# Kernel optimization log

Hardware: AMD Instinct MI355X
Metric: run time of the kernel (lower is better)

The kernel has to match this reference:

```python
import jax, jax.numpy as jnp
import numpy as np

B, T, F, H, K = 64, 256, 16, 128, 3


def setup_inputs() -> dict:
    key = jax.random.key(0)
    ks = jax.random.split(key, 8)
    s = 1.0 / np.sqrt(H)
    x = jax.random.normal(ks[0], (B, T, F), jnp.float32)
    index = jnp.sort(jax.random.randint(ks[1], (B, 2), 0, T), axis=1)
    # per-feature LSTM params (input dim 1), torch gate order [i, f, g, o]
    W_ih = jax.random.uniform(ks[2], (F, 4 * H), jnp.float32, -s, s)
    W_hh = jax.random.uniform(ks[3], (F, 4 * H, H), jnp.float32, -s, s)
    b = jax.random.uniform(ks[4], (F, 4 * H), jnp.float32, -s, s)  # b_ih + b_hh folded
    conv_w = jax.random.uniform(ks[5], (K,), jnp.float32, -1.0 / np.sqrt(K), 1.0 / np.sqrt(K))
    fc_w = jax.random.uniform(ks[6], (F * H, 2), jnp.float32, -1.0 / np.sqrt(F * H), 1.0 / np.sqrt(F * H))
    fc_b = jax.random.uniform(ks[7], (2,), jnp.float32, -1.0 / np.sqrt(F * H), 1.0 / np.sqrt(F * H))
    return dict(x=x, index=index, W_ih=W_ih, W_hh=W_hh, b=b, conv_w=conv_w, fc_w=fc_w, fc_b=fc_b)


def reference(x, index, W_ih, W_hh, b, conv_w, fc_w, fc_b):
    Bn, Tn, Fn = x.shape
    Hn = W_hh.shape[-1]
    t = jnp.arange(Tn)
    # valid[b, t] = start <= t < end; recurrence only advances inside the ragged slice
    valid = (t[None, :] >= index[:, 0:1]) & (t[None, :] < index[:, 1:2])  # [B, T]
    xs = jnp.moveaxis(x, 1, 0)            # [T, B, F]
    ms = jnp.moveaxis(valid, 1, 0)[:, :, None, None]  # [T, B, 1, 1]

    def step(carry, inp):
        h, c = carry                       # [B, F, H] each
        x_t, m = inp                       # [B, F], [B, 1, 1]
        gates = x_t[:, :, None] * W_ih[None] \
            + jnp.einsum('bfh,fgh->bfg', h, W_hh) + b[None]  # [B, F, 4H]
        i, f, g, o = jnp.split(gates, 4, axis=-1)
        i = jax.nn.sigmoid(i); f = jax.nn.sigmoid(f)
        g = jnp.tanh(g); o = jax.nn.sigmoid(o)
        c_new = f * c + i * g
        h_new = o * jnp.tanh(c_new)
        h = jnp.where(m, h_new, h)
        c = jnp.where(m, c_new, c)
        return (h, c), None

    h0 = jnp.zeros((Bn, Fn, Hn), x.dtype)
    (h, _), _ = jax.lax.scan(step, (h0, h0), (xs, ms))
    outs = h                               # [B, F, H] == last LSTM output per slice

    cofs = outs.mean(axis=-1)              # AdaptiveAvgPool1d(1) -> [B, F]
    cofs = jax.lax.conv_general_dilated(
        cofs[:, None, :], conv_w[None, None, :], (1,), [(K // 2, K // 2)],
        dimension_numbers=('NCH', 'OIH', 'NCH'))[:, 0, :]  # [B, F]
    gate = jax.nn.sigmoid(cofs)
    outs = outs * gate[:, :, None]
    return outs.reshape(Bn, -1) @ fc_w + fc_b  # [B, 2]
```

## Files before the change

### kernel.cpp

```cpp
#include <hip/hip_runtime.h>

typedef _Float16 half_t;
typedef half_t half2_t __attribute__((ext_vector_type(2)));
typedef half_t half8  __attribute__((ext_vector_type(8)));
typedef unsigned int uint_t;
typedef uint_t uint4v __attribute__((ext_vector_type(4)));
typedef float float4v __attribute__((ext_vector_type(4)));

#define B_  64
#define T_  256
#define F_  16
#define H_  128
#define HP  160
#define LOG2E 1.44269504f

__device__ __forceinline__ float rcp_(float x)  { return __builtin_amdgcn_rcpf(x); }
__device__ __forceinline__ float sigm2(float x) { return rcp_(1.0f + __builtin_amdgcn_exp2f(x * -LOG2E)); }
__device__ __forceinline__ float tanh2(float x) { return fmaf(rcp_(1.0f + __builtin_amdgcn_exp2f(x * (-2.0f * LOG2E))), 2.0f, -1.0f); }
__device__ __forceinline__ float sigm(float x)  { return rcp_(1.0f + __expf(-x)); }

__global__ void make_sched(const int* __restrict__ index, int* __restrict__ pairs) {
    __shared__ int ss[B_], ee[B_], mid[B_], bo[B_];
    const int t = threadIdx.x;
    const int s = index[2 * t], e = index[2 * t + 1];
    ss[t] = s; ee[t] = e; mid[t] = s + e;
    __syncthreads();
    int m = mid[t], r = 0;
    for (int j = 0; j < B_; ++j) r += (mid[j] < m) || (mid[j] == m && j < t);
    bo[r] = t;
    __syncthreads();
    if (t < 32) {
        int bA = bo[2 * t], bB = bo[2 * t + 1];
        int su = min(ss[bA], ss[bB]), eu = max(ee[bA], ee[bB]);
        int4 v;
        v.x = (bA << 8) | bB;
        v.y = (ss[bA] << 16) | ee[bA];
        v.z = (ss[bB] << 16) | ee[bB];
        v.w = (su << 16) | eu;
        ((int4*)pairs)[t] = v;
    }
}

__global__ void repack_w(const float* __restrict__ whh, uint_t* __restrict__ wt) {
    const int f = blockIdx.x, w = blockIdx.y, tid = threadIdx.x;
    const int lane = tid & 63, q4 = tid >> 6;
    const int li = lane & 15, lg = lane >> 4;
    const float* base = whh + (size_t)f * 512 * 128;
#pragma unroll
    for (int qq = 0; qq < 4; ++qq) {
        const int qf = q4 * 4 + qq;
        const int m = qf >> 2, kt = qf & 3;
        const int g512 = 128 * m + 16 * w + li;
        uint_t tmp[4];
#pragma unroll
        for (int e2 = 0; e2 < 4; ++e2) {
            int k = kt * 32 + lg * 8 + 2 * e2;
            half2_t h;
            h[0] = (half_t)base[g512 * 128 + k];
            h[1] = (half_t)base[g512 * 128 + k + 1];
            tmp[e2] = __builtin_bit_cast(uint_t, h);
        }
        uint4 out = { tmp[0], tmp[1], tmp[2], tmp[3] };
        ((uint4*)wt)[(((size_t)f * 8 + w) * 16 + qf) * 64 + lane] = out;
    }
}

__global__ __launch_bounds__(512, 4) void lstm_mfma(
    const float* __restrict__ x, const uint_t* __restrict__ wt,
    const float* __restrict__ wih_g, const float* __restrict__ bias_g,
    const int* __restrict__ pairs, float* __restrict__ hout)
{
    __shared__ float xsh[2][T_ + 8];
    __shared__ alignas(16) half_t hbuf[2][2][HP];

    const int f = blockIdx.x & 15;
    const int4 pv = ((const int4*)pairs)[blockIdx.x >> 4];
    const int bA = pv.x >> 8, bB = pv.x & 255;
    const int sA = pv.y >> 16, eA = pv.y & 0xffff;
    const int sB = pv.z >> 16, eB = pv.z & 0xffff;
    const int su = pv.w >> 16, eu = pv.w & 0xffff;

    const int tid = threadIdx.x, lane = tid & 63, w = tid >> 6;
    const int li = lane & 15, lg = lane >> 4;
    const int cell = 16 * w + li;
    const int hsel = li >> 3;
    const int csel = lg >> 1;

    uint4v wr[16];
    {
        const char* ws = (const char*)wt + ((((size_t)f * 8 + w) * 16) * 64 + lane) * 16;
#pragma unroll
        for (int q = 0; q < 16; ++q) {
            unsigned long long a = (unsigned long long)(ws + (size_t)q * 1024);
            asm volatile("global_load_dwordx4 %0, %1, off" : "=v"(wr[q]) : "v"(a));
        }
        asm volatile("s_waitcnt vmcnt(0)");
        __builtin_amdgcn_sched_barrier(0);
    }

    float wih[4], bb4[4];
#pragma unroll
    for (int m = 0; m < 4; ++m) {
        wih[m] = wih_g[f * 512 + 128 * m + cell];
        bb4[m] = bias_g[f * 512 + 128 * m + cell];
    }

    const int myb = csel ? bB : bA;
    const int mys = csel ? sB : sA;
    const int mye = csel ? eB : eA;

    {
        int bb_ = tid >> 8, tt = tid & 255;
        xsh[bb_][tt] = x[((size_t)(bb_ ? bB : bA) * T_ + tt) * F_ + f];
    }
    if (tid < 2 * H_) hbuf[0][tid >> 7][tid & 127] = (half_t)0.0f;

    float cst = 0.0f, hst = 0.0f;
    int pp = 0;
    __syncthreads();

    for (int t = su; t < eu; ++t) {
        const half_t* hb = &hbuf[pp][hsel][lg * 8];
        half8 a0 = *(const half8*)(hb + 0);
        half8 a1 = *(const half8*)(hb + 32);
        half8 a2 = *(const half8*)(hb + 64);
        half8 a3 = *(const half8*)(hb + 96);
        float xt = xsh[csel][t];

        float gv[4];
#pragma unroll
        for (int m = 0; m < 4; ++m) {
            float iv = fmaf(xt, wih[m], bb4[m]);
            float4v ci = { iv, iv, iv, iv };
            ci = __builtin_amdgcn_mfma_f32_16x16x32_f16(a0, __builtin_bit_cast(half8, wr[m * 4 + 0]), ci, 0, 0, 0);
            ci = __builtin_amdgcn_mfma_f32_16x16x32_f16(a1, __builtin_bit_cast(half8, wr[m * 4 + 1]), ci, 0, 0, 0);
            ci = __builtin_amdgcn_mfma_f32_16x16x32_f16(a2, __builtin_bit_cast(half8, wr[m * 4 + 2]), ci, 0, 0, 0);
            ci = __builtin_amdgcn_mfma_f32_16x16x32_f16(a3, __builtin_bit_cast(half8, wr[m * 4 + 3]), ci, 0, 0, 0);
            gv[m] = ci[0];
        }

        float gi = sigm2(gv[0]);
        float gf = sigm2(gv[1]);
        float gg = tanh2(gv[2]);
        float go = sigm2(gv[3]);
        float cn = fmaf(gf, cst, gi * gg);
        bool mk = (t >= mys) & (t < mye);
        cst = mk ? cn : cst;
        float hn = go * tanh2(cst);
        hst = mk ? hn : hst;

        if ((lg & 1) == 0) hbuf[pp ^ 1][csel][cell] = (half_t)hst;
        __syncthreads();
        pp ^= 1;
    }

    if ((lg & 1) == 0) hout[((size_t)myb * F_ + f) * H_ + cell] = hst;
}

__global__ void epilogue(const float* __restrict__ hout, const float* __restrict__ conv_w,
                         const float* __restrict__ fc_w, const float* __restrict__ fc_b,
                         float* __restrict__ out)
{
    const int b = blockIdx.x, t = threadIdx.x;
    const int lane = t & 63, wv = t >> 6;
    __shared__ float part[2][16];
    __shared__ float gate_sh[16];

    float hv[16];
#pragma unroll
    for (int f = 0; f < 16; ++f) hv[f] = hout[((size_t)b * 16 + f) * 128 + t];

#pragma unroll
    for (int f = 0; f < 16; ++f) {
        float s = hv[f];
#pragma unroll
        for (int off = 32; off >= 1; off >>= 1) s += __shfl_down(s, off, 64);
        if (lane == 0) part[wv][f] = s;
    }
    __syncthreads();
    if (t < 16) gate_sh[t] = (part[0][t] + part[1][t]) * (1.0f / 128.0f);
    __syncthreads();
    float gate = 0.0f;
    if (t < 16) {
        float l  = (t > 0)  ? gate_sh[t - 1] : 0.0f;
        float mi = gate_sh[t];
        float r  = (t < 15) ? gate_sh[t + 1] : 0.0f;
        gate = sigm(fmaf(l, conv_w[0], fmaf(mi, conv_w[1], r * conv_w[2])));
    }
    __syncthreads();
    if (t < 16) gate_sh[t] = gate;
    __syncthreads();

    float acc0 = 0.0f, acc1 = 0.0f;
    const float2* fw2 = (const float2*)fc_w;
#pragma unroll
    for (int f = 0; f < 16; ++f) {
        float hg = hv[f] * gate_sh[f];
        float2 w2 = fw2[f * 128 + t];
        acc0 = fmaf(hg, w2.x, acc0);
        acc1 = fmaf(hg, w2.y, acc1);
    }
#pragma unroll
    for (int off = 32; off >= 1; off >>= 1) {
        acc0 += __shfl_down(acc0, off, 64);
        acc1 += __shfl_down(acc1, off, 64);
    }
    if (lane == 0) { part[wv][0] = acc0; part[wv][1] = acc1; }
    __syncthreads();
    if (t == 0) {
        out[b * 2 + 0] = part[0][0] + part[1][0] + fc_b[0];
        out[b * 2 + 1] = part[0][1] + part[1][1] + fc_b[1];
    }
}

extern "C" void kernel_launch(void* const* d_in, const int* in_sizes, int n_in,
                              void* d_out, int out_size, void* d_ws, size_t ws_size,
                              hipStream_t stream) {
    const float* x      = (const float*)d_in[0];
    const int*   index  = (const int*)  d_in[1];
    const float* W_ih   = (const float*)d_in[2];
    const float* W_hh   = (const float*)d_in[3];
    const float* bias   = (const float*)d_in[4];
    const float* conv_w = (const float*)d_in[5];
    const float* fc_w   = (const float*)d_in[6];
    const float* fc_b   = (const float*)d_in[7];
    float* out = (float*)d_out;

    uint_t* wt    = (uint_t*)d_ws;
    float*  hout  = (float*)((char*)d_ws + 2 * 1024 * 1024);
    int*    pairs = (int*)((char*)d_ws + 2 * 1024 * 1024 + 512 * 1024);

    make_sched<<<1, 64, 0, stream>>>(index, pairs);
    repack_w<<<dim3(F_, 8), 256, 0, stream>>>(W_hh, wt);
    lstm_mfma<<<512, 512, 0, stream>>>(x, wt, W_ih, bias, pairs, hout);
    epilogue<<<B_, 128, 0, stream>>>(hout, conv_w, fc_w, fc_b, out);
}
```

Measured before the change: 136.0 us.

## Halve LSTM block size by giving each wave two cell tiles

Each block now runs 4 waves instead of 8, and each wave handles two 16-cell column tiles, holding twice as many weight registers and issuing 32 MFMAs per step. The input and bias term is added after the MFMA chain instead of seeding the accumulator. Every lane then writes a distinct hidden value, so no lanes sit idle on the store. The aim is to cut the per-step barrier cost, since fewer waves synchronise each timestep. In exchange each wave does twice the serial MFMA and activation work, register pressure rises, and occupancy may drop.

```diff
diff --git a/kernel.cpp b/kernel.cpp
--- a/kernel.cpp
+++ b/kernel.cpp
@@ -65,7 +65,7 @@
     }
 }
 
-__global__ __launch_bounds__(512, 4) void lstm_mfma(
+__global__ __launch_bounds__(256, 2) void lstm_mfma(
     const float* __restrict__ x, const uint_t* __restrict__ wt,
     const float* __restrict__ wih_g, const float* __restrict__ bias_g,
     const int* __restrict__ pairs, float* __restrict__ hout)
@@ -82,40 +82,50 @@
 
     const int tid = threadIdx.x, lane = tid & 63, w = tid >> 6;
     const int li = lane & 15, lg = lane >> 4;
-    const int cell = 16 * w + li;
     const int hsel = li >> 3;
     const int csel = lg >> 1;
-
-    uint4v wr[16];
+    const int sub  = lg & 1;
+    const int cell0 = 16 * w + li;
+    const int wcell = cell0 + 64 * sub;
+
+    uint4v wr[2][16];
     {
-        const char* ws = (const char*)wt + ((((size_t)f * 8 + w) * 16) * 64 + lane) * 16;
-#pragma unroll
-        for (int q = 0; q < 16; ++q) {
-            unsigned long long a = (unsigned long long)(ws + (size_t)q * 1024);
-            asm volatile("global_load_dwordx4 %0, %1, off" : "=v"(wr[q]) : "v"(a));
+#pragma unroll
+        for (int cb = 0; cb < 2; ++cb) {
+            const char* ws = (const char*)wt + ((((size_t)f * 8 + (w + 4 * cb)) * 16) * 64 + lane) * 16;
+#pragma unroll
+            for (int q = 0; q < 16; ++q) {
+                unsigned long long a = (unsigned long long)(ws + (size_t)q * 1024);
+                asm volatile("global_load_dwordx4 %0, %1, off" : "=v"(wr[cb][q]) : "v"(a));
+            }
         }
         asm volatile("s_waitcnt vmcnt(0)");
         __builtin_amdgcn_sched_barrier(0);
     }
 
-    float wih[4], bb4[4];
-#pragma unroll
-    for (int m = 0; m < 4; ++m) {
-        wih[m] = wih_g[f * 512 + 128 * m + cell];
-        bb4[m] = bias_g[f * 512 + 128 * m + cell];
-    }
+    float wih[2][4], bb4[2][4];
+#pragma unroll
+    for (int cb = 0; cb < 2; ++cb)
+#pragma unroll
+        for (int m = 0; m < 4; ++m) {
+            wih[cb][m] = wih_g[f * 512 + 128 * m + cell0 + 64 * cb];
+            bb4[cb][m] = bias_g[f * 512 + 128 * m + cell0 + 64 * cb];
+        }
 
     const int myb = csel ? bB : bA;
     const int mys = csel ? sB : sA;
     const int mye = csel ? eB : eA;
 
-    {
-        int bb_ = tid >> 8, tt = tid & 255;
+#pragma unroll
+    for (int j = 0; j < 2; ++j) {
+        int idx = tid + 256 * j;
+        int bb_ = idx >> 8, tt = idx & 255;
         xsh[bb_][tt] = x[((size_t)(bb_ ? bB : bA) * T_ + tt) * F_ + f];
     }
     if (tid < 2 * H_) hbuf[0][tid >> 7][tid & 127] = (half_t)0.0f;
 
-    float cst = 0.0f, hst = 0.0f;
+    float cst[2] = {0.f, 0.f}, hst[2] = {0.f, 0.f};
+    const float4v z4 = {0.f, 0.f, 0.f, 0.f};
     int pp = 0;
     __syncthreads();
 
@@ -127,34 +137,38 @@
         half8 a3 = *(const half8*)(hb + 96);
         float xt = xsh[csel][t];
 
-        float gv[4];
-#pragma unroll
-        for (int m = 0; m < 4; ++m) {
-            float iv = fmaf(xt, wih[m], bb4[m]);
-            float4v ci = { iv, iv, iv, iv };
-            ci = __builtin_amdgcn_mfma_f32_16x16x32_f16(a0, __builtin_bit_cast(half8, wr[m * 4 + 0]), ci, 0, 0, 0);
-            ci = __builtin_amdgcn_mfma_f32_16x16x32_f16(a1, __builtin_bit_cast(half8, wr[m * 4 + 1]), ci, 0, 0, 0);
-            ci = __builtin_amdgcn_mfma_f32_16x16x32_f16(a2, __builtin_bit_cast(half8, wr[m * 4 + 2]), ci, 0, 0, 0);
-            ci = __builtin_amdgcn_mfma_f32_16x16x32_f16(a3, __builtin_bit_cast(half8, wr[m * 4 + 3]), ci, 0, 0, 0);
-            gv[m] = ci[0];
-        }
-
-        float gi = sigm2(gv[0]);
-        float gf = sigm2(gv[1]);
-        float gg = tanh2(gv[2]);
-        float go = sigm2(gv[3]);
-        float cn = fmaf(gf, cst, gi * gg);
+        float gv[2][4];
+#pragma unroll
+        for (int cb = 0; cb < 2; ++cb)
+#pragma unroll
+            for (int m = 0; m < 4; ++m) {
+                float4v ci;
+                ci = __builtin_amdgcn_mfma_f32_16x16x32_f16(a0, __builtin_bit_cast(half8, wr[cb][m * 4 + 0]), z4, 0, 0, 0);
+                ci = __builtin_amdgcn_mfma_f32_16x16x32_f16(a1, __builtin_bit_cast(half8, wr[cb][m * 4 + 1]), ci, 0, 0, 0);
+                ci = __builtin_amdgcn_mfma_f32_16x16x32_f16(a2, __builtin_bit_cast(half8, wr[cb][m * 4 + 2]), ci, 0, 0, 0);
+                ci = __builtin_amdgcn_mfma_f32_16x16x32_f16(a3, __builtin_bit_cast(half8, wr[cb][m * 4 + 3]), ci, 0, 0, 0);
+                gv[cb][m] = ci[0] + fmaf(xt, wih[cb][m], bb4[cb][m]);
+            }
+
         bool mk = (t >= mys) & (t < mye);
-        cst = mk ? cn : cst;
-        float hn = go * tanh2(cst);
-        hst = mk ? hn : hst;
-
-        if ((lg & 1) == 0) hbuf[pp ^ 1][csel][cell] = (half_t)hst;
+#pragma unroll
+        for (int cb = 0; cb < 2; ++cb) {
+            float gi = sigm2(gv[cb][0]);
+            float gf = sigm2(gv[cb][1]);
+            float gg = tanh2(gv[cb][2]);
+            float go = sigm2(gv[cb][3]);
+            float cn = fmaf(gf, cst[cb], gi * gg);
+            cst[cb] = mk ? cn : cst[cb];
+            float hn = go * tanh2(cst[cb]);
+            hst[cb] = mk ? hn : hst[cb];
+        }
+
+        hbuf[pp ^ 1][csel][wcell] = (half_t)hst[sub];
         __syncthreads();
         pp ^= 1;
     }
 
-    if ((lg & 1) == 0) hout[((size_t)myb * F_ + f) * H_ + cell] = hst;
+    hout[((size_t)myb * F_ + f) * H_ + wcell] = hst[sub];
 }
 
 __global__ void epilogue(const float* __restrict__ hout, const float* __restrict__ conv_w,
@@ -232,6 +246,6 @@
 
     make_sched<<<1, 64, 0, stream>>>(index, pairs);
     repack_w<<<dim3(F_, 8), 256, 0, stream>>>(W_hh, wt);
-    lstm_mfma<<<512, 512, 0, stream>>>(x, wt, W_ih, bias, pairs, hout);
+    lstm_mfma<<<512, 256, 0, stream>>>(x, wt, W_ih, bias, pairs, hout);
     epilogue<<<B_, 128, 0, stream>>>(hout, conv_w, fc_w, fc_b, out);
 }
```

After: 150.0 us. 1.1x slower.

## Sort batch pairs by span length, split MFMA chains, and peel mask-free loop

Applied to the files above, without the earlier changes.

The schedule kernel now sorts batch pairs by union length, longest first, and interleaves the block-to-pair mapping so long recurrences are dispatched first, which evens out tail imbalance across CUs. Each gate's four-deep dependent MFMA chain is split into two independent two-deep chains that are summed, shortening the serial latency per timestep. The time loop is peeled into masked head and tail segments and an unmasked middle where both batches are active, removing select logic from the common case. This costs some code size and an extra add per gate, and slightly changes fp summation order.

```diff
diff --git a/kernel.cpp b/kernel.cpp
--- a/kernel.cpp
+++ b/kernel.cpp
@@ -21,6 +21,8 @@
 
 __global__ void make_sched(const int* __restrict__ index, int* __restrict__ pairs) {
     __shared__ int ss[B_], ee[B_], mid[B_], bo[B_];
+    __shared__ int pu[32];
+    __shared__ int4 praw[32];
     const int t = threadIdx.x;
     const int s = index[2 * t], e = index[2 * t + 1];
     ss[t] = s; ee[t] = e; mid[t] = s + e;
@@ -37,7 +39,13 @@
         v.y = (ss[bA] << 16) | ee[bA];
         v.z = (ss[bB] << 16) | ee[bB];
         v.w = (su << 16) | eu;
-        ((int4*)pairs)[t] = v;
+        praw[t] = v; pu[t] = eu - su;
+    }
+    __syncthreads();
+    if (t < 32) {
+        int u = pu[t], r2 = 0;
+        for (int j = 0; j < 32; ++j) r2 += (pu[j] > u) || (pu[j] == u && j < t);
+        ((int4*)pairs)[r2] = praw[t];
     }
 }
 
@@ -73,8 +81,9 @@
     __shared__ float xsh[2][T_ + 8];
     __shared__ alignas(16) half_t hbuf[2][2][HP];
 
-    const int f = blockIdx.x & 15;
-    const int4 pv = ((const int4*)pairs)[blockIdx.x >> 4];
+    const int lo = blockIdx.x & 255, hi = blockIdx.x >> 8;
+    const int f = lo & 15, g = lo >> 4;
+    const int4 pv = ((const int4*)pairs)[2 * g + hi];
     const int bA = pv.x >> 8, bB = pv.x & 255;
     const int sA = pv.y >> 16, eA = pv.y & 0xffff;
     const int sB = pv.z >> 16, eB = pv.z & 0xffff;
@@ -116,10 +125,11 @@
     if (tid < 2 * H_) hbuf[0][tid >> 7][tid & 127] = (half_t)0.0f;
 
     float cst = 0.0f, hst = 0.0f;
+    const float4v z4 = {0.f, 0.f, 0.f, 0.f};
     int pp = 0;
     __syncthreads();
 
-    for (int t = su; t < eu; ++t) {
+    auto step = [&](int t, bool do_mask) {
         const half_t* hb = &hbuf[pp][hsel][lg * 8];
         half8 a0 = *(const half8*)(hb + 0);
         half8 a1 = *(const half8*)(hb + 32);
@@ -130,13 +140,11 @@
         float gv[4];
 #pragma unroll
         for (int m = 0; m < 4; ++m) {
-            float iv = fmaf(xt, wih[m], bb4[m]);
-            float4v ci = { iv, iv, iv, iv };
-            ci = __builtin_amdgcn_mfma_f32_16x16x32_f16(a0, __builtin_bit_cast(half8, wr[m * 4 + 0]), ci, 0, 0, 0);
-            ci = __builtin_amdgcn_mfma_f32_16x16x32_f16(a1, __builtin_bit_cast(half8, wr[m * 4 + 1]), ci, 0, 0, 0);
-            ci = __builtin_amdgcn_mfma_f32_16x16x32_f16(a2, __builtin_bit_cast(half8, wr[m * 4 + 2]), ci, 0, 0, 0);
-            ci = __builtin_amdgcn_mfma_f32_16x16x32_f16(a3, __builtin_bit_cast(half8, wr[m * 4 + 3]), ci, 0, 0, 0);
-            gv[m] = ci[0];
+            float4v ca = __builtin_amdgcn_mfma_f32_16x16x32_f16(a0, __builtin_bit_cast(half8, wr[m * 4 + 0]), z4, 0, 0, 0);
+            float4v cb = __builtin_amdgcn_mfma_f32_16x16x32_f16(a1, __builtin_bit_cast(half8, wr[m * 4 + 1]), z4, 0, 0, 0);
+            ca = __builtin_amdgcn_mfma_f32_16x16x32_f16(a2, __builtin_bit_cast(half8, wr[m * 4 + 2]), ca, 0, 0, 0);
+            cb = __builtin_amdgcn_mfma_f32_16x16x32_f16(a3, __builtin_bit_cast(half8, wr[m * 4 + 3]), cb, 0, 0, 0);
+            gv[m] = (ca[0] + cb[0]) + fmaf(xt, wih[m], bb4[m]);
         }
 
         float gi = sigm2(gv[0]);
@@ -144,15 +152,27 @@
         float gg = tanh2(gv[2]);
         float go = sigm2(gv[3]);
         float cn = fmaf(gf, cst, gi * gg);
-        bool mk = (t >= mys) & (t < mye);
-        cst = mk ? cn : cst;
-        float hn = go * tanh2(cst);
-        hst = mk ? hn : hst;
+        if (do_mask) {
+            bool mk = (t >= mys) & (t < mye);
+            cst = mk ? cn : cst;
+            float hn = go * tanh2(cst);
+            hst = mk ? hn : hst;
+        } else {
+            cst = cn;
+            hst = go * tanh2(cst);
+        }
 
         if ((lg & 1) == 0) hbuf[pp ^ 1][csel][cell] = (half_t)hst;
         __syncthreads();
         pp ^= 1;
-    }
+    };
+
+    int p1 = min(max(sA, sB), eu);
+    int p2 = max(min(eA, eB), p1);
+    int t = su;
+    for (; t < p1; ++t) step(t, true);
+    for (; t < p2; ++t) step(t, false);
+    for (; t < eu; ++t) step(t, true);
 
     if ((lg & 1) == 0) hout[((size_t)myb * F_ + f) * H_ + cell] = hst;
 }
```

After: 170.7 us. +25.5%, slower.
